# Optimization experiments

Measured on AMD Instinct MI355X. Metric: run time of the kernel, lower is better.

The kernel has to match this reference:

```python
import jax, jax.numpy as jnp
import numpy as np

B, S, D = 2048, 200, 128   # batch, n_steps, embedding dim per vector
H = 64                      # hidden_dim
MASK_SCALE = 1e10


def setup_inputs() -> dict:
    key = jax.random.key(0)
    ks = jax.random.split(key, 6)
    his = jax.random.normal(ks[0], (B, S, D), dtype=jnp.float32)
    target = jax.random.normal(ks[1], (B, 1, D), dtype=jnp.float32)
    # mask == 1.0 marks padded history positions (they get -1e10 added pre-softmax)
    mask = (jax.random.uniform(ks[2], (B, S)) < 0.3).astype(jnp.float32)
    W = jax.random.normal(ks[3], (3 * D, H), dtype=jnp.float32) * 0.1
    W_bias = jnp.full((H,), 0.1, dtype=jnp.float32)
    O = jax.random.normal(ks[4], (H, 1), dtype=jnp.float32) * 0.1
    O_bias = jnp.full((1,), 0.1, dtype=jnp.float32)
    return {"his": his, "target": target, "mask": mask,
            "W": W, "W_bias": W_bias, "O": O, "O_bias": O_bias}


def reference(his, target, mask, W, W_bias, O, O_bias):
    tgt = jnp.broadcast_to(target, his.shape)          # [B,S,D] tile over steps
    diff = his - tgt
    att_vec = jnp.concatenate([his, diff, tgt], axis=2)  # [B,S,3D]
    h = jax.nn.relu(jnp.einsum('bsf,fh->bsh', att_vec, W) + W_bias)  # [B,S,H]
    alpha = jnp.einsum('bsh,ho->bso', h, O) + O_bias   # [B,S,1]
    alpha = alpha[:, :, 0] - mask * MASK_SCALE         # [B,S]
    attn = jax.nn.softmax(alpha, axis=-1)              # [B,S]
    out = jnp.einsum('bs,bsd->bd', attn, his)          # weighted-sum pooling
    return out
```

## Files before the change

### kernel.cpp

```cpp
#include <hip/hip_runtime.h>

#define B_ 2048
#define S_ 200
#define D_ 128
#define H_ 64
#define ROWS (B_ * S_)
#define MASK_SCALE 1e10f

typedef __attribute__((ext_vector_type(8))) short short8_t;
typedef __attribute__((ext_vector_type(4))) float f32x4;

__device__ __forceinline__ short f2bf(float f) {
    unsigned u = __float_as_uint(f);
    unsigned r = (u + 0x7fffu + ((u >> 16) & 1u)) >> 16;
    return (short)r;
}

__global__ __launch_bounds__(256) void prep_w(const float* __restrict__ W,
                                              float* __restrict__ wt,
                                              unsigned short* __restrict__ wfrag) {
    for (int idx = threadIdx.x; idx < D_ * H_; idx += 256) {
        int d = idx >> 6;
        int h = idx & 63;
        float w1 = W[d * H_ + h];
        float w2 = W[(D_ + d) * H_ + h];
        float w3 = W[(2 * D_ + d) * H_ + h];
        wt[idx] = w3 - w2;
        int kt = d >> 5, q = (d >> 3) & 3, j = d & 7;
        int nt = h >> 4, lm = h & 15;
        int lane = (q << 4) | lm;
        wfrag[((kt * 4 + nt) * 64 + lane) * 8 + j] = (unsigned short)f2bf(w1 + w2);
    }
}

__global__ __launch_bounds__(64) void prep_tproj(const float* __restrict__ target,
                                                 const float* __restrict__ W_bias,
                                                 const float* __restrict__ wt,
                                                 float* __restrict__ tproj) {
    int b = blockIdx.x;
    int h = threadIdx.x;
    float acc = W_bias[h];
    const float* tg = target + (size_t)b * D_;
    #pragma unroll 8
    for (int d = 0; d < D_; ++d)
        acc = fmaf(tg[d], wt[d * H_ + h], acc);
    tproj[b * H_ + h] = acc;
}

__global__ __launch_bounds__(256) void alpha_kernel(const float* __restrict__ his,
                                                    const float* __restrict__ mask,
                                                    const unsigned short* __restrict__ wfrag,
                                                    const float* __restrict__ tproj,
                                                    const float* __restrict__ Ovec,
                                                    const float* __restrict__ O_bias,
                                                    float* __restrict__ alpha) {
    const int lane = threadIdx.x & 63;
    const int wv = threadIdx.x >> 6;
    const int tile = blockIdx.x * 4 + wv;
    const int row0 = tile * 16;
    const int lm = lane & 15;
    const int q = lane >> 4;

    short8_t bfrag[16];
    #pragma unroll
    for (int f = 0; f < 16; ++f)
        bfrag[f] = *(const short8_t*)(wfrag + ((size_t)(f * 64 + lane)) * 8);

    f32x4 acc[4];
    #pragma unroll
    for (int nt = 0; nt < 4; ++nt) acc[nt] = (f32x4){0.f, 0.f, 0.f, 0.f};

    const int arow = row0 + lm;
    const float* hp = his + (size_t)arow * D_ + q * 8;

    #pragma unroll
    for (int kt = 0; kt < 4; ++kt) {
        float4 x0 = *(const float4*)(hp + kt * 32);
        float4 x1 = *(const float4*)(hp + kt * 32 + 4);
        short8_t a;
        a[0] = f2bf(x0.x); a[1] = f2bf(x0.y); a[2] = f2bf(x0.z); a[3] = f2bf(x0.w);
        a[4] = f2bf(x1.x); a[5] = f2bf(x1.y); a[6] = f2bf(x1.z); a[7] = f2bf(x1.w);
        #pragma unroll
        for (int nt = 0; nt < 4; ++nt)
            acc[nt] = __builtin_amdgcn_mfma_f32_16x16x32_bf16(a, bfrag[kt * 4 + nt], acc[nt], 0, 0, 0);
    }

    float part[4];
    #pragma unroll
    for (int r = 0; r < 4; ++r) {
        int grow = row0 + q * 4 + r;
        int b = grow / S_;
        float sum = 0.f;
        #pragma unroll
        for (int nt = 0; nt < 4; ++nt) {
            int h = nt * 16 + lm;
            float v = acc[nt][r] + tproj[b * H_ + h];
            v = fmaxf(v, 0.f);
            sum = fmaf(v, Ovec[h], sum);
        }
        part[r] = sum;
    }
    #pragma unroll
    for (int off = 1; off < 16; off <<= 1) {
        #pragma unroll
        for (int r = 0; r < 4; ++r)
            part[r] += __shfl_xor(part[r], off);
    }
    if (lm == 0) {
        float ob = O_bias[0];
        #pragma unroll
        for (int r = 0; r < 4; ++r) {
            int grow = row0 + q * 4 + r;
            alpha[grow] = part[r] + ob - mask[grow] * MASK_SCALE;
        }
    }
}

__global__ __launch_bounds__(256) void pool_kernel(const float* __restrict__ his,
                                                   const float* __restrict__ alpha,
                                                   float* __restrict__ out) {
    __shared__ float sred[256];
    __shared__ float wgt[S_];
    __shared__ float partial[D_];

    const int b = blockIdx.x;
    const int t = threadIdx.x;

    float a = (t < S_) ? alpha[b * S_ + t] : -INFINITY;
    sred[t] = a;
    __syncthreads();
    #pragma unroll
    for (int s = 128; s > 0; s >>= 1) {
        if (t < s) sred[t] = fmaxf(sred[t], sred[t + s]);
        __syncthreads();
    }
    float m = sred[0];
    __syncthreads();
    float e = (t < S_) ? expf(a - m) : 0.f;
    sred[t] = e;
    __syncthreads();
    #pragma unroll
    for (int s = 128; s > 0; s >>= 1) {
        if (t < s) sred[t] += sred[t + s];
        __syncthreads();
    }
    float inv = 1.f / sred[0];
    if (t < S_) wgt[t] = e * inv;
    __syncthreads();

    const int d = t & 127;
    const int half = t >> 7;
    const float* hb = his + (size_t)b * S_ * D_ + (size_t)half * 100 * D_ + d;
    float accv = 0.f;
    #pragma unroll 4
    for (int s = 0; s < 100; ++s)
        accv = fmaf(wgt[half * 100 + s], hb[(size_t)s * D_], accv);

    if (half) partial[d] = accv;
    __syncthreads();
    if (!half) out[b * D_ + d] = accv + partial[d];
}

extern "C" void kernel_launch(void* const* d_in, const int* in_sizes, int n_in,
                              void* d_out, int out_size, void* d_ws, size_t ws_size,
                              hipStream_t stream) {
    const float* his    = (const float*)d_in[0];
    const float* target = (const float*)d_in[1];
    const float* mask   = (const float*)d_in[2];
    const float* W      = (const float*)d_in[3];
    const float* W_bias = (const float*)d_in[4];
    const float* Ovec   = (const float*)d_in[5];
    const float* O_bias = (const float*)d_in[6];
    float* out = (float*)d_out;

    char* ws = (char*)d_ws;
    float* wt             = (float*)(ws);
    unsigned short* wfrag = (unsigned short*)(ws + 32768);
    float* tproj          = (float*)(ws + 65536);
    float* alpha          = (float*)(ws + 65536 + 524288);

    prep_w<<<1, 256, 0, stream>>>(W, wt, wfrag);
    prep_tproj<<<B_, 64, 0, stream>>>(target, W_bias, wt, tproj);
    alpha_kernel<<<ROWS / 64, 256, 0, stream>>>(his, mask, wfrag, tproj, Ovec, O_bias, alpha);
    pool_kernel<<<B_, 256, 0, stream>>>(his, alpha, out);
}
```

Baseline: 342.7 us.

## Fuse alpha MLP, softmax and pooling into one per-batch kernel with LDS-staged bf16 history

Replaces the separate alpha and pooling kernels with one block per batch row. The block loads the history once into LDS as bf16, runs the MFMA projection from LDS, does a shuffle-based softmax, and pools from the same LDS copy. This removes the second full read of the history tensor and the alpha round trip through global memory. O_bias is dropped because softmax is shift-invariant. Pooling now uses bf16-rounded history values, which lowers output precision, and the large LDS footprint limits occupancy.

```diff
diff --git a/kernel.cpp b/kernel.cpp
--- a/kernel.cpp
+++ b/kernel.cpp
@@ -4,16 +4,20 @@
 #define S_ 200
 #define D_ 128
 #define H_ 64
-#define ROWS (B_ * S_)
 #define MASK_SCALE 1e10f
+#define LSTRIDE 136
 
 typedef __attribute__((ext_vector_type(8))) short short8_t;
 typedef __attribute__((ext_vector_type(4))) float f32x4;
-
-__device__ __forceinline__ short f2bf(float f) {
+typedef __attribute__((ext_vector_type(4))) unsigned short ushort4_t;
+
+__device__ __forceinline__ unsigned short f2bf(float f) {
     unsigned u = __float_as_uint(f);
     unsigned r = (u + 0x7fffu + ((u >> 16) & 1u)) >> 16;
-    return (short)r;
+    return (unsigned short)r;
+}
+__device__ __forceinline__ float bf2f(unsigned short v) {
+    return __uint_as_float(((unsigned)v) << 16);
 }
 
 __global__ __launch_bounds__(256) void prep_w(const float* __restrict__ W,
@@ -29,7 +33,7 @@
         int kt = d >> 5, q = (d >> 3) & 3, j = d & 7;
         int nt = h >> 4, lm = h & 15;
         int lane = (q << 4) | lm;
-        wfrag[((kt * 4 + nt) * 64 + lane) * 8 + j] = (unsigned short)f2bf(w1 + w2);
+        wfrag[((kt * 4 + nt) * 64 + lane) * 8 + j] = f2bf(w1 + w2);
     }
 }
 
@@ -47,118 +51,135 @@
     tproj[b * H_ + h] = acc;
 }
 
-__global__ __launch_bounds__(256) void alpha_kernel(const float* __restrict__ his,
-                                                    const float* __restrict__ mask,
-                                                    const unsigned short* __restrict__ wfrag,
-                                                    const float* __restrict__ tproj,
-                                                    const float* __restrict__ Ovec,
-                                                    const float* __restrict__ O_bias,
-                                                    float* __restrict__ alpha) {
-    const int lane = threadIdx.x & 63;
-    const int wv = threadIdx.x >> 6;
-    const int tile = blockIdx.x * 4 + wv;
-    const int row0 = tile * 16;
-    const int lm = lane & 15;
-    const int q = lane >> 4;
+__global__ __launch_bounds__(256, 2) void fused_kernel(const float* __restrict__ his,
+                                                       const float* __restrict__ mask,
+                                                       const unsigned short* __restrict__ wfrag,
+                                                       const float* __restrict__ tproj,
+                                                       const float* __restrict__ Ovec,
+                                                       float* __restrict__ out) {
+    __shared__ unsigned short hisb[S_ * LSTRIDE];
+    __shared__ float alpha_s[208];
+    __shared__ float red8[8];
+    __shared__ float tp_s[H_];
+    __shared__ float ov_s[H_];
+    __shared__ float pool_s[3 * D_];
+
+    const int b    = blockIdx.x;
+    const int t    = threadIdx.x;
+    const int lane = t & 63;
+    const int wv   = t >> 6;
+    const int lm   = lane & 15;
+    const int q    = lane >> 4;
 
     short8_t bfrag[16];
     #pragma unroll
     for (int f = 0; f < 16; ++f)
         bfrag[f] = *(const short8_t*)(wfrag + ((size_t)(f * 64 + lane)) * 8);
 
-    f32x4 acc[4];
-    #pragma unroll
-    for (int nt = 0; nt < 4; ++nt) acc[nt] = (f32x4){0.f, 0.f, 0.f, 0.f};
-
-    const int arow = row0 + lm;
-    const float* hp = his + (size_t)arow * D_ + q * 8;
-
-    #pragma unroll
-    for (int kt = 0; kt < 4; ++kt) {
-        float4 x0 = *(const float4*)(hp + kt * 32);
-        float4 x1 = *(const float4*)(hp + kt * 32 + 4);
-        short8_t a;
-        a[0] = f2bf(x0.x); a[1] = f2bf(x0.y); a[2] = f2bf(x0.z); a[3] = f2bf(x0.w);
-        a[4] = f2bf(x1.x); a[5] = f2bf(x1.y); a[6] = f2bf(x1.z); a[7] = f2bf(x1.w);
-        #pragma unroll
-        for (int nt = 0; nt < 4; ++nt)
-            acc[nt] = __builtin_amdgcn_mfma_f32_16x16x32_bf16(a, bfrag[kt * 4 + nt], acc[nt], 0, 0, 0);
-    }
-
-    float part[4];
-    #pragma unroll
-    for (int r = 0; r < 4; ++r) {
-        int grow = row0 + q * 4 + r;
-        int b = grow / S_;
-        float sum = 0.f;
-        #pragma unroll
-        for (int nt = 0; nt < 4; ++nt) {
-            int h = nt * 16 + lm;
-            float v = acc[nt][r] + tproj[b * H_ + h];
-            v = fmaxf(v, 0.f);
-            sum = fmaf(v, Ovec[h], sum);
-        }
-        part[r] = sum;
-    }
-    #pragma unroll
-    for (int off = 1; off < 16; off <<= 1) {
-        #pragma unroll
-        for (int r = 0; r < 4; ++r)
-            part[r] += __shfl_xor(part[r], off);
-    }
-    if (lm == 0) {
-        float ob = O_bias[0];
+    if (t < H_) {
+        tp_s[t] = tproj[b * H_ + t];
+        ov_s[t] = Ovec[t];
+    }
+
+    const float4* hb4 = (const float4*)(his + (size_t)b * S_ * D_);
+    #pragma unroll
+    for (int i = t, it = 0; it < (S_ * D_ / 4 + 255) / 256; ++it, i += 256) {
+        if (i < S_ * D_ / 4) {
+            float4 x = hb4[i];
+            int s  = i >> 5;
+            int d4 = i & 31;
+            ushort4_t v;
+            v[0] = f2bf(x.x); v[1] = f2bf(x.y); v[2] = f2bf(x.z); v[3] = f2bf(x.w);
+            *(ushort4_t*)(&hisb[s * LSTRIDE + d4 * 4]) = v;
+        }
+    }
+    __syncthreads();
+
+    for (int tile = wv; tile < 13; tile += 4) {
+        int row0 = tile * 16;
+        int ar = row0 + lm; if (ar > S_ - 1) ar = S_ - 1;
+        const unsigned short* ap = &hisb[ar * LSTRIDE + q * 8];
+
+        f32x4 acc[4];
+        #pragma unroll
+        for (int nt = 0; nt < 4; ++nt) acc[nt] = (f32x4){0.f, 0.f, 0.f, 0.f};
+
+        #pragma unroll
+        for (int kt = 0; kt < 4; ++kt) {
+            short8_t a = *(const short8_t*)(ap + kt * 32);
+            #pragma unroll
+            for (int nt = 0; nt < 4; ++nt)
+                acc[nt] = __builtin_amdgcn_mfma_f32_16x16x32_bf16(a, bfrag[kt * 4 + nt], acc[nt], 0, 0, 0);
+        }
+
+        float part[4];
         #pragma unroll
         for (int r = 0; r < 4; ++r) {
-            int grow = row0 + q * 4 + r;
-            alpha[grow] = part[r] + ob - mask[grow] * MASK_SCALE;
-        }
-    }
-}
-
-__global__ __launch_bounds__(256) void pool_kernel(const float* __restrict__ his,
-                                                   const float* __restrict__ alpha,
-                                                   float* __restrict__ out) {
-    __shared__ float sred[256];
-    __shared__ float wgt[S_];
-    __shared__ float partial[D_];
-
-    const int b = blockIdx.x;
-    const int t = threadIdx.x;
-
-    float a = (t < S_) ? alpha[b * S_ + t] : -INFINITY;
-    sred[t] = a;
-    __syncthreads();
-    #pragma unroll
-    for (int s = 128; s > 0; s >>= 1) {
-        if (t < s) sred[t] = fmaxf(sred[t], sred[t + s]);
-        __syncthreads();
-    }
-    float m = sred[0];
-    __syncthreads();
-    float e = (t < S_) ? expf(a - m) : 0.f;
-    sred[t] = e;
-    __syncthreads();
-    #pragma unroll
-    for (int s = 128; s > 0; s >>= 1) {
-        if (t < s) sred[t] += sred[t + s];
-        __syncthreads();
-    }
-    float inv = 1.f / sred[0];
-    if (t < S_) wgt[t] = e * inv;
-    __syncthreads();
-
-    const int d = t & 127;
-    const int half = t >> 7;
-    const float* hb = his + (size_t)b * S_ * D_ + (size_t)half * 100 * D_ + d;
-    float accv = 0.f;
-    #pragma unroll 4
-    for (int s = 0; s < 100; ++s)
-        accv = fmaf(wgt[half * 100 + s], hb[(size_t)s * D_], accv);
-
-    if (half) partial[d] = accv;
-    __syncthreads();
-    if (!half) out[b * D_ + d] = accv + partial[d];
+            float sum = 0.f;
+            #pragma unroll
+            for (int nt = 0; nt < 4; ++nt) {
+                int h = nt * 16 + lm;
+                float v = acc[nt][r] + tp_s[h];
+                v = fmaxf(v, 0.f);
+                sum = fmaf(v, ov_s[h], sum);
+            }
+            part[r] = sum;
+        }
+        #pragma unroll
+        for (int off = 1; off < 16; off <<= 1) {
+            #pragma unroll
+            for (int r = 0; r < 4; ++r)
+                part[r] += __shfl_xor(part[r], off);
+        }
+        if (lm == 0) {
+            #pragma unroll
+            for (int r = 0; r < 4; ++r)
+                alpha_s[row0 + q * 4 + r] = part[r];
+        }
+    }
+    __syncthreads();
+
+    float a = (t < S_) ? alpha_s[t] - mask[(size_t)b * S_ + t] * MASK_SCALE : -INFINITY;
+    float m = a;
+    #pragma unroll
+    for (int off = 1; off < 64; off <<= 1) m = fmaxf(m, __shfl_xor(m, off));
+    if (lane == 0) red8[wv] = m;
+    __syncthreads();
+    m = fmaxf(fmaxf(red8[0], red8[1]), fmaxf(red8[2], red8[3]));
+    float e = (t < S_) ? __expf(a - m) : 0.f;
+    float ssum = e;
+    #pragma unroll
+    for (int off = 1; off < 64; off <<= 1) ssum += __shfl_xor(ssum, off);
+    if (lane == 0) red8[4 + wv] = ssum;
+    __syncthreads();
+    float inv = 1.f / (red8[4] + red8[5] + red8[6] + red8[7]);
+    __syncthreads();
+    if (t < S_) alpha_s[t] = e * inv;
+    __syncthreads();
+
+    const int d2 = t & 63;
+    const int sg = t >> 6;
+    float ax = 0.f, ay = 0.f;
+    for (int s = sg; s < S_; s += 4) {
+        float w = alpha_s[s];
+        unsigned v = *(const unsigned*)(&hisb[s * LSTRIDE + d2 * 2]);
+        ax = fmaf(w, bf2f((unsigned short)(v & 0xffff)), ax);
+        ay = fmaf(w, bf2f((unsigned short)(v >> 16)), ay);
+    }
+    if (sg) {
+        pool_s[(sg - 1) * D_ + d2 * 2]     = ax;
+        pool_s[(sg - 1) * D_ + d2 * 2 + 1] = ay;
+    }
+    __syncthreads();
+    if (sg == 0) {
+        #pragma unroll
+        for (int k = 0; k < 3; ++k) {
+            ax += pool_s[k * D_ + d2 * 2];
+            ay += pool_s[k * D_ + d2 * 2 + 1];
+        }
+        float2 o; o.x = ax; o.y = ay;
+        ((float2*)out)[b * (D_ / 2) + d2] = o;
+    }
 }
 
 extern "C" void kernel_launch(void* const* d_in, const int* in_sizes, int n_in,
@@ -170,17 +191,14 @@
     const float* W      = (const float*)d_in[3];
     const float* W_bias = (const float*)d_in[4];
     const float* Ovec   = (const float*)d_in[5];
-    const float* O_bias = (const float*)d_in[6];
     float* out = (float*)d_out;
 
     char* ws = (char*)d_ws;
     float* wt             = (float*)(ws);
     unsigned short* wfrag = (unsigned short*)(ws + 32768);
     float* tproj          = (float*)(ws + 65536);
-    float* alpha          = (float*)(ws + 65536 + 524288);
 
     prep_w<<<1, 256, 0, stream>>>(W, wt, wfrag);
     prep_tproj<<<B_, 64, 0, stream>>>(target, W_bias, wt, tproj);
-    alpha_kernel<<<ROWS / 64, 256, 0, stream>>>(his, mask, wfrag, tproj, Ovec, O_bias, alpha);
-    pool_kernel<<<B_, 256, 0, stream>>>(his, alpha, out);
-}
+    fused_kernel<<<B_, 256, 0, stream>>>(his, mask, wfrag, tproj, Ovec, out);
+}
```

Result: faster. 328.2 us (-4.2%).
